# Optimization experiments

Measured on AMD Instinct MI355X. Metric: run time of the kernel, lower is better.

The kernel has to match this reference:

```python
import jax, jax.numpy as jnp
import numpy as np

DIFF = 16  # static enlargement (max shake amplitude), offsets lie in [0, DIFF]


def setup_inputs() -> dict:
    key = jax.random.key(0)
    k1, k2, k3 = jax.random.split(key, 3)
    B, C, T, H, W = 8, 3, 32, 224, 224
    video = jax.random.uniform(k1, (B, C, T, H, W), dtype=jnp.float32)
    shake_h = jax.random.randint(k2, (T,), 0, DIFF + 1, dtype=jnp.int32)
    shake_w = jax.random.randint(k3, (T,), 0, DIFF + 1, dtype=jnp.int32)
    return {"video": video, "shake_h": shake_h, "shake_w": shake_w}


def reference(video, shake_h, shake_w):
    # Faithful jax version of Transform_Camera.forward_shake with the
    # randomly sampled shake curve provided as (already normalized)
    # per-frame integer offsets shake_h, shake_w in [0, DIFF].
    B, C, T, H, W = video.shape
    Hb, Wb = H + DIFF, W + DIFF
    # trilinear upsample over (T, H, W), half-pixel centers == torch align_corners=False
    enlarged = jax.image.resize(video, (B, C, T, Hb, Wb), method="trilinear")
    enlarged = jnp.clip(enlarged, 0.0, 1.0)

    def crop(frame, h, w):
        # frame: [B, C, Hb, Wb]; per-frame varying crop of size HxW
        return jax.lax.dynamic_slice(frame, (0, 0, h, w), (B, C, H, W))

    # vmap over the T axis replaces the python loop of crops + stack
    out = jax.vmap(crop, in_axes=(2, 0, 0), out_axes=2)(enlarged, shake_h, shake_w)
    return out  # [B, C, T, H, W]
```

## Files before the change

### kernel.cpp

```cpp
#include <hip/hip_runtime.h>

#define NB 8
#define NC 3
#define NT 32
#define NH 224
#define NW 224
#define DIFF 16
#define INV_SCALE (224.0f / 240.0f)

#define TILE_ROWS 16
#define LDS_ROWS 16
#define TILES_PER_FRAME (NH / TILE_ROWS)
#define NFRAMES (NB * NC * NT)

__global__ __launch_bounds__(256) void shake_crop_col_kernel(
    const float* __restrict__ video,
    const int* __restrict__ shake_h,
    const int* __restrict__ shake_w,
    float* __restrict__ out)
{
    __shared__ float lds[LDS_ROWS * NW];

    const int tid  = threadIdx.x;
    const int f    = blockIdx.x / TILES_PER_FRAME;
    const int tile = blockIdx.x % TILES_PER_FRAME;
    const int t    = f % NT;
    const int ybase = tile * TILE_ROWS;

    const int sh = shake_h[t];
    const int sw = shake_w[t];

    float iy_first = fminf(fmaxf((ybase + sh + 0.5f) * INV_SCALE - 0.5f, 0.0f), (float)(NH - 1));
    float iy_last  = fminf(fmaxf((ybase + TILE_ROWS - 1 + sh + 0.5f) * INV_SCALE - 0.5f, 0.0f), (float)(NH - 1));
    const int r0    = (int)iy_first;
    const int r_end = min((int)iy_last + 1, NH - 1);
    const int nrows = r_end - r0 + 1;

    const float* frame = video + (size_t)f * (NH * NW);
    const float4* src4 = (const float4*)(frame + r0 * NW);
    float4* lds4 = (float4*)lds;
    const int n4 = nrows * (NW / 4);
    for (int j = tid; j < n4; j += 256)
        lds4[j] = src4[j];
    __syncthreads();

    const int x = tid;
    if (x >= NW) return;

    float ix = fminf(fmaxf((x + sw + 0.5f) * INV_SCALE - 0.5f, 0.0f), (float)(NW - 1));
    int   x0 = (int)ix;
    float fx = ix - (float)x0;
    int   x1 = min(x0 + 1, NW - 1);

    float* ocol = out + (size_t)f * (NH * NW) + (size_t)ybase * NW + x;

    #pragma unroll
    for (int ry = 0; ry < TILE_ROWS; ++ry) {
        float iy = fminf(fmaxf((ybase + ry + sh + 0.5f) * INV_SCALE - 0.5f, 0.0f), (float)(NH - 1));
        int   y0 = (int)iy;
        float fy = iy - (float)y0;
        int   y1 = min(y0 + 1, NH - 1);
        const float* row0 = lds + (y0 - r0) * NW;
        const float* row1 = lds + (y1 - r0) * NW;

        float v00 = row0[x0];
        float v01 = row0[x1];
        float v10 = row1[x0];
        float v11 = row1[x1];

        float top = v00 + fx * (v01 - v00);
        float bot = v10 + fx * (v11 - v10);
        float v   = top + fy * (bot - top);
        ocol[(size_t)ry * NW] = fminf(fmaxf(v, 0.0f), 1.0f);
    }
}

extern "C" void kernel_launch(void* const* d_in, const int* in_sizes, int n_in,
                              void* d_out, int out_size, void* d_ws, size_t ws_size,
                              hipStream_t stream) {
    const float* video   = (const float*)d_in[0];
    const int*   shake_h = (const int*)d_in[1];
    const int*   shake_w = (const int*)d_in[2];
    float*       out     = (float*)d_out;

    const int grid = NFRAMES * TILES_PER_FRAME;
    shake_crop_col_kernel<<<grid, 256, 0, stream>>>(video, shake_h, shake_w, out);
}
```

Measured before the change: 267.6 us.

## Use persistent grid with double-buffered async global-to-LDS tile staging

```diff
diff --git a/kernel.cpp b/kernel.cpp
--- a/kernel.cpp
+++ b/kernel.cpp
@@ -12,66 +12,110 @@
 #define LDS_ROWS 16
 #define TILES_PER_FRAME (NH / TILE_ROWS)
 #define NFRAMES (NB * NC * NT)
+#define NTILES (NFRAMES * TILES_PER_FRAME)
+#define GRID 1280
 
-__global__ __launch_bounds__(256) void shake_crop_col_kernel(
+struct TileParams {
+    int f;
+    int sh, sw;
+    int ybase;
+    int rbase;
+};
+
+__device__ __forceinline__ TileParams tile_params(int tile, const int* sh_l, const int* sw_l)
+{
+    TileParams p;
+    p.f = tile / TILES_PER_FRAME;
+    const int tl = tile - p.f * TILES_PER_FRAME;
+    const int t  = p.f % NT;
+    p.sh = sh_l[t];
+    p.sw = sw_l[t];
+    p.ybase = tl * TILE_ROWS;
+    float iy0 = fminf(fmaxf((p.ybase + p.sh + 0.5f) * INV_SCALE - 0.5f, 0.0f), (float)(NH - 1));
+    int r0 = (int)iy0;
+    p.rbase = min(r0, NH - LDS_ROWS);
+    return p;
+}
+
+__device__ __forceinline__ void stage_tile(const float* __restrict__ video,
+                                           const TileParams& p, float* buf, int tid)
+{
+    const float* src = video + (size_t)p.f * (NH * NW) + (size_t)p.rbase * NW;
+    #pragma unroll
+    for (int k = 0; k < 4; ++k) {
+        int j = tid + k * 256;
+        if (j < LDS_ROWS * NW / 4) {
+            __builtin_amdgcn_global_load_lds(
+                (const __attribute__((address_space(1))) void*)(src + j * 4),
+                (__attribute__((address_space(3))) void*)(buf + j * 4),
+                16, 0, 0);
+        }
+    }
+}
+
+__global__ __launch_bounds__(256) void shake_crop_pipe_kernel(
     const float* __restrict__ video,
     const int* __restrict__ shake_h,
     const int* __restrict__ shake_w,
     float* __restrict__ out)
 {
-    __shared__ float lds[LDS_ROWS * NW];
+    __shared__ float lds[2][LDS_ROWS * NW];
+    __shared__ int sh_l[NT], sw_l[NT];
 
-    const int tid  = threadIdx.x;
-    const int f    = blockIdx.x / TILES_PER_FRAME;
-    const int tile = blockIdx.x % TILES_PER_FRAME;
-    const int t    = f % NT;
-    const int ybase = tile * TILE_ROWS;
-
-    const int sh = shake_h[t];
-    const int sw = shake_w[t];
-
-    float iy_first = fminf(fmaxf((ybase + sh + 0.5f) * INV_SCALE - 0.5f, 0.0f), (float)(NH - 1));
-    float iy_last  = fminf(fmaxf((ybase + TILE_ROWS - 1 + sh + 0.5f) * INV_SCALE - 0.5f, 0.0f), (float)(NH - 1));
-    const int r0    = (int)iy_first;
-    const int r_end = min((int)iy_last + 1, NH - 1);
-    const int nrows = r_end - r0 + 1;
-
-    const float* frame = video + (size_t)f * (NH * NW);
-    const float4* src4 = (const float4*)(frame + r0 * NW);
-    float4* lds4 = (float4*)lds;
-    const int n4 = nrows * (NW / 4);
-    for (int j = tid; j < n4; j += 256)
-        lds4[j] = src4[j];
+    const int tid = threadIdx.x;
+    if (tid < NT) { sh_l[tid] = shake_h[tid]; sw_l[tid] = shake_w[tid]; }
     __syncthreads();
 
-    const int x = tid;
-    if (x >= NW) return;
+    int tile0 = blockIdx.x;
+    TileParams cur = tile_params(tile0, sh_l, sw_l);
+    stage_tile(video, cur, &lds[0][0], tid);
+    __syncthreads();
 
-    float ix = fminf(fmaxf((x + sw + 0.5f) * INV_SCALE - 0.5f, 0.0f), (float)(NW - 1));
-    int   x0 = (int)ix;
-    float fx = ix - (float)x0;
-    int   x1 = min(x0 + 1, NW - 1);
+    int p = 0;
+    for (int t = tile0; t < NTILES; t += GRID) {
+        const int nxt = t + GRID;
+        TileParams np = cur;
+        if (nxt < NTILES) {
+            np = tile_params(nxt, sh_l, sw_l);
+            stage_tile(video, np, &lds[p ^ 1][0], tid);
+        }
 
-    float* ocol = out + (size_t)f * (NH * NW) + (size_t)ybase * NW + x;
+        const float* buf = &lds[p][0];
+        if (tid < NW) {
+            const int x = tid;
+            float ix = fminf(fmaxf((x + cur.sw + 0.5f) * INV_SCALE - 0.5f, 0.0f), (float)(NW - 1));
+            int   x0 = (int)ix;
+            float fx = ix - (float)x0;
+            int   x1 = min(x0 + 1, NW - 1);
 
-    #pragma unroll
-    for (int ry = 0; ry < TILE_ROWS; ++ry) {
-        float iy = fminf(fmaxf((ybase + ry + sh + 0.5f) * INV_SCALE - 0.5f, 0.0f), (float)(NH - 1));
-        int   y0 = (int)iy;
-        float fy = iy - (float)y0;
-        int   y1 = min(y0 + 1, NH - 1);
-        const float* row0 = lds + (y0 - r0) * NW;
-        const float* row1 = lds + (y1 - r0) * NW;
+            float* ocol = out + (size_t)cur.f * (NH * NW) + (size_t)cur.ybase * NW + x;
+            const int ys = cur.ybase + cur.sh;
 
-        float v00 = row0[x0];
-        float v01 = row0[x1];
-        float v10 = row1[x0];
-        float v11 = row1[x1];
+            #pragma unroll
+            for (int ry = 0; ry < TILE_ROWS; ++ry) {
+                float iy = fminf(fmaxf((ys + ry + 0.5f) * INV_SCALE - 0.5f, 0.0f), (float)(NH - 1));
+                int   y0 = (int)iy;
+                float fy = iy - (float)y0;
+                int   y1 = min(y0 + 1, NH - 1);
+                const float* row0 = buf + (y0 - cur.rbase) * NW;
+                const float* row1 = buf + (y1 - cur.rbase) * NW;
 
-        float top = v00 + fx * (v01 - v00);
-        float bot = v10 + fx * (v11 - v10);
-        float v   = top + fy * (bot - top);
-        ocol[(size_t)ry * NW] = fminf(fmaxf(v, 0.0f), 1.0f);
+                float v00 = row0[x0];
+                float v01 = row0[x1];
+                float v10 = row1[x0];
+                float v11 = row1[x1];
+
+                float top = v00 + fx * (v01 - v00);
+                float bot = v10 + fx * (v11 - v10);
+                float v   = top + fy * (bot - top);
+                ocol[(size_t)ry * NW] = fminf(fmaxf(v, 0.0f), 1.0f);
+            }
+        }
+
+        __syncthreads();
+
+        cur = np;
+        p ^= 1;
     }
 }
 
@@ -83,6 +127,5 @@
     const int*   shake_w = (const int*)d_in[2];
     float*       out     = (float*)d_out;
 
-    const int grid = NFRAMES * TILES_PER_FRAME;
-    shake_crop_col_kernel<<<grid, 256, 0, stream>>>(video, shake_h, shake_w, out);
+    shake_crop_pipe_kernel<<<GRID, 256, 0, stream>>>(video, shake_h, shake_w, out);
 }
```

After: 269.4 us. Within noise of the previous version (+0.7%).
